# Optimization experiments

Measured on AMD Instinct MI355X. Metric: run time of the kernel, lower is better.

Reference implementation:

```python
import jax, jax.numpy as jnp
import numpy as np

B, S, H = 4, 1024, 2048
NQ, NKV, D = 32, 4, 128
EPS = 1e-6
THETA = 1e6


def setup_inputs() -> dict:
    key = jax.random.key(0)
    k1, k2, k3 = jax.random.split(key, 3)
    hidden = jax.random.normal(k1, (B, S, H), jnp.float32) * 0.02
    w_qkv = jax.random.normal(k2, (H, (NQ + 2 * NKV) * D), jnp.float32) * 0.02
    w_o = jax.random.normal(k3, (NQ * D, H), jnp.float32) * 0.02
    q_norm_w = jnp.ones((D,), jnp.float32)
    k_norm_w = jnp.ones((D,), jnp.float32)
    # rotary tables, broadcast to [B, S, D]
    inv_freq = 1.0 / (THETA ** (jnp.arange(0, D, 2, dtype=jnp.float32) / D))
    freqs = jnp.arange(S, dtype=jnp.float32)[:, None] * inv_freq[None, :]  # [S, D/2]
    emb = jnp.concatenate([freqs, freqs], axis=-1)  # [S, D]
    cos = jnp.broadcast_to(jnp.cos(emb)[None], (B, S, D))
    sin = jnp.broadcast_to(jnp.sin(emb)[None], (B, S, D))
    return {"hidden": hidden, "w_qkv": w_qkv, "w_o": w_o,
            "q_norm_w": q_norm_w, "k_norm_w": k_norm_w, "cos": cos, "sin": sin}


def _rms_norm(x, w):
    xf = x.astype(jnp.float32)
    var = jnp.mean(xf * xf, axis=-1, keepdims=True)
    return (w * (xf * jax.lax.rsqrt(var + EPS))).astype(x.dtype)


def _rotate_half(x):
    h = x.shape[-1] // 2
    return jnp.concatenate([-x[..., h:], x[..., :h]], axis=-1)


def reference(hidden, w_qkv, w_o, q_norm_w, k_norm_w, cos, sin):
    b, s, _ = hidden.shape
    qkv = jnp.einsum('bsh,he->bse', hidden, w_qkv)
    q = qkv[..., : NQ * D].reshape(b, s, NQ, D)
    k = qkv[..., NQ * D: (NQ + NKV) * D].reshape(b, s, NKV, D)
    v = qkv[..., (NQ + NKV) * D:].reshape(b, s, NKV, D)

    # per-head RMSNorm on Q and K
    q = _rms_norm(q, q_norm_w)
    k = _rms_norm(k, k_norm_w)

    # fused RoPE (rotate-half), cos/sin broadcast over heads
    c = cos[:, :, None, :]
    sn = sin[:, :, None, :]
    q = q * c + _rotate_half(q) * sn
    k = k * c + _rotate_half(k) * sn

    # GQA causal flash-attention (prefill, sparse_mode=3 -> causal)
    g = NQ // NKV
    qg = q.reshape(b, s, NKV, g, D)
    scale = 1.0 / jnp.sqrt(jnp.asarray(D, hidden.dtype))
    scores = jnp.einsum('bqkgd,bskd->bkgqs', qg, k) * scale  # [B,NKV,g,S,S]
    causal = jnp.tril(jnp.ones((s, s), bool))
    scores = jnp.where(causal[None, None, None], scores, jnp.finfo(scores.dtype).min)
    probs = jax.nn.softmax(scores, axis=-1)
    out = jnp.einsum('bkgqs,bskd->bqkgd', probs, v).reshape(b, s, NQ * D)
    return jnp.einsum('bse,eh->bsh', out, w_o)
```

## Files before the change

### kernel.cpp

```cpp
#include <hip/hip_runtime.h>

#define BB 4
#define SS 1024
#define HH 2048
#define NQH 32
#define NKVH 4
#define DD 128
#define EQKV 5120

typedef __attribute__((ext_vector_type(8))) short s8v;
typedef __attribute__((ext_vector_type(4))) short s4v;
typedef __attribute__((ext_vector_type(4))) float f4v;

__device__ __forceinline__ unsigned short f2bf(float f) {
  unsigned int u = __builtin_bit_cast(unsigned int, f);
  u += 0x7fffu + ((u >> 16) & 1u);
  return (unsigned short)(u >> 16);
}
__device__ __forceinline__ float bf2f(unsigned short s) {
  unsigned int u = ((unsigned int)s) << 16;
  return __builtin_bit_cast(float, u);
}

__device__ __forceinline__ void async16(unsigned short* lds, const unsigned short* g) {
  __builtin_amdgcn_global_load_lds(
      (const __attribute__((address_space(1))) unsigned int*)g,
      (__attribute__((address_space(3))) unsigned int*)lds, 16, 0, 0);
}


__global__ __launch_bounds__(256) void cvt_bf16(const float* __restrict__ in,
                                                unsigned short* __restrict__ out, int n) {
  int i = (blockIdx.x * 256 + threadIdx.x) * 4;
  if (i >= n) return;
  f4v v = *reinterpret_cast<const f4v*>(in + i);
  s4v o;
#pragma unroll
  for (int j = 0; j < 4; ++j) o[j] = (short)f2bf(v[j]);
  *reinterpret_cast<s4v*>(out + i) = o;
}

__global__ __launch_bounds__(256) void transpose_cvt(const float* __restrict__ in,
                                                     unsigned short* __restrict__ out,
                                                     int K, int N) {
  __shared__ unsigned short T[64][65];
  const int k0 = blockIdx.y * 64, n0 = blockIdx.x * 64;
  const int t = threadIdx.x;
  const int r = t >> 4, c4 = (t & 15) * 4;
#pragma unroll
  for (int i = 0; i < 4; ++i) {
    f4v v = *reinterpret_cast<const f4v*>(&in[(size_t)(k0 + r + i * 16) * N + n0 + c4]);
#pragma unroll
    for (int j = 0; j < 4; ++j) T[r + i * 16][c4 + j] = f2bf(v[j]);
  }
  __syncthreads();
#pragma unroll
  for (int i = 0; i < 4; ++i) {
    int n = r + i * 16;
    s4v o;
#pragma unroll
    for (int j = 0; j < 4; ++j) o[j] = (short)T[c4 + j][n];
    *reinterpret_cast<s4v*>(&out[(size_t)(n0 + n) * K + k0 + c4]) = o;
  }
}

__global__ __launch_bounds__(256) void vtrans(const unsigned short* __restrict__ qkv,
                                              unsigned short* __restrict__ Vt) {
  __shared__ unsigned short T[64][68];
  const int s0 = blockIdx.x * 64;
  const int d0 = blockIdx.y * 64;
  const int bk = blockIdx.z;
  const int b = bk >> 2, hkv = bk & 3;
  const int t = threadIdx.x;
  const int r = t >> 4, c4 = (t & 15) * 4;
  const unsigned short* src = qkv + (size_t)(b * SS + s0) * EQKV + (NQH + NKVH + hkv) * DD + d0;
#pragma unroll
  for (int i = 0; i < 4; ++i) {
    int s = r + i * 16;
    s4v v = *reinterpret_cast<const s4v*>(src + (size_t)s * EQKV + c4);
    *reinterpret_cast<s4v*>(&T[s][c4]) = v;
  }
  __syncthreads();
#pragma unroll
  for (int i = 0; i < 4; ++i) {
    int d = r + i * 16;
    s4v o;
#pragma unroll
    for (int j = 0; j < 4; ++j) o[j] = (short)T[c4 + j][d];
    *reinterpret_cast<s4v*>(&Vt[((size_t)bk * DD + d0 + d) * SS + s0 + c4]) = o;
  }
}

template <bool CF32>
__global__ __launch_bounds__(256) void gemm_bt(const unsigned short* __restrict__ A,
                                               const unsigned short* __restrict__ Bt,
                                               void* __restrict__ Cp,
                                               int M, int N, int K, int lda) {
  __shared__ unsigned short As[128 * 32];
  __shared__ unsigned short Bs[128 * 32];
  const int tid = threadIdx.x;
  const int ln = tid & 63, wv = tid >> 6;
  const int la = ln & 15, quad = ln >> 4;
  const int m0 = blockIdx.y * 128, n0 = blockIdx.x * 128;
  const int wm = (wv >> 1) * 64, wn = (wv & 1) * 64;
  f4v acc[4][4] = {};

  const int srow = wv * 16 + (ln >> 2);
  const int scol = (ln & 3) * 8;
  const unsigned short* Ab = A + (size_t)(m0 + srow) * lda + scol;
  const unsigned short* Bb = Bt + (size_t)(n0 + srow) * K + scol;
  unsigned short* AsW = &As[wv * 16 * 32];
  unsigned short* BsW = &Bs[wv * 16 * 32];

  for (int k0 = 0; k0 < K; k0 += 32) {
    async16(AsW,           Ab + k0);
    async16(AsW + 64 * 32, Ab + (size_t)64 * lda + k0);
    async16(BsW,           Bb + k0);
    async16(BsW + 64 * 32, Bb + (size_t)64 * K + k0);
    __syncthreads();
    s8v af[4], bf[4];
#pragma unroll
    for (int mi = 0; mi < 4; ++mi)
      af[mi] = *reinterpret_cast<const s8v*>(&As[(wm + mi * 16 + la) * 32 + quad * 8]);
#pragma unroll
    for (int ni = 0; ni < 4; ++ni)
      bf[ni] = *reinterpret_cast<const s8v*>(&Bs[(wn + ni * 16 + la) * 32 + quad * 8]);
#pragma unroll
    for (int mi = 0; mi < 4; ++mi)
#pragma unroll
      for (int ni = 0; ni < 4; ++ni)
        acc[mi][ni] = __builtin_amdgcn_mfma_f32_16x16x32_bf16(af[mi], bf[ni], acc[mi][ni], 0, 0, 0);
    __syncthreads();
  }
#pragma unroll
  for (int mi = 0; mi < 4; ++mi)
#pragma unroll
    for (int ni = 0; ni < 4; ++ni)
#pragma unroll
      for (int r = 0; r < 4; ++r) {
        int row = m0 + wm + mi * 16 + quad * 4 + r;
        int col = n0 + wn + ni * 16 + la;
        if constexpr (CF32) ((float*)Cp)[(size_t)row * N + col] = acc[mi][ni][r];
        else ((unsigned short*)Cp)[(size_t)row * N + col] = f2bf(acc[mi][ni][r]);
      }
}

__global__ __launch_bounds__(256) void attn2(unsigned short* __restrict__ qkv,
                                             const unsigned short* __restrict__ Vt) {
  const int idx = blockIdx.x;
  const int tile = 15 - (idx >> 7);
  const int h = idx & 31;
  const int b = (idx >> 5) & 3;
  const int hkv = h >> 3;
  const int tid = threadIdx.x;
  const int ln = tid & 63, w = tid >> 6;
  const int la = ln & 15, quad = ln >> 4;
  const int qr0 = tile * 64;
  __shared__ unsigned short Ks[64 * 128];
  __shared__ unsigned short Vts[128 * 64];
  __shared__ unsigned short Ps[4][16][64];

  const size_t rowb = (size_t)b * SS;
  s8v qf[4];
  {
    const unsigned short* qrow = qkv + (rowb + qr0 + w * 16 + la) * EQKV + h * DD;
#pragma unroll
    for (int t = 0; t < 4; ++t) qf[t] = *reinterpret_cast<const s8v*>(qrow + t * 32 + quad * 8);
  }
  const unsigned short* kcol = qkv + (NQH + hkv) * DD;
  const unsigned short* vtb = Vt + (size_t)(b * NKVH + hkv) * DD * SS;

  float m_[4], l_[4], al[4];
  f4v acc[8] = {};
#pragma unroll
  for (int r = 0; r < 4; ++r) { m_[r] = -1.0e30f; l_[r] = 0.f; }

  const float scale = 0.08838834764831845f;
  const int nkb = tile + 1;
  for (int kb = 0; kb < nkb; ++kb) {
    const int key0 = kb * 64;
    __syncthreads();
#pragma unroll
    for (int i = 0; i < 4; ++i) {
      int row = w * 16 + i * 4 + (ln >> 4);
      int chunk = (ln & 15) ^ (row & 15);
      async16(&Ks[(w * 16 + i * 4) * 128],
              kcol + (rowb + key0 + row) * EQKV + chunk * 8);
    }
#pragma unroll
    for (int i = 0; i < 4; ++i) {
      int row = w * 32 + i * 8 + (ln >> 3);
      int chunk = (ln & 7) ^ (ln >> 3);
      async16(&Vts[(w * 32 + i * 8) * 64],
              vtb + (size_t)row * SS + key0 + chunk * 8);
    }
    __syncthreads();
    f4v sc[4];
#pragma unroll
    for (int kt = 0; kt < 4; ++kt) {
      f4v z = {};
#pragma unroll
      for (int t = 0; t < 4; ++t) {
        s8v kf = *reinterpret_cast<const s8v*>(&Ks[(kt * 16 + la) * 128 + ((t * 4 + quad) ^ la) * 8]);
        z = __builtin_amdgcn_mfma_f32_16x16x32_bf16(qf[t], kf, z, 0, 0, 0);
      }
      sc[kt] = z;
    }
    const bool diag = (kb == nkb - 1);
#pragma unroll
    for (int r = 0; r < 4; ++r) {
      float v[4];
      if (diag) {
        int q = qr0 + w * 16 + quad * 4 + r;
#pragma unroll
        for (int kt = 0; kt < 4; ++kt)
          v[kt] = (key0 + kt * 16 + la <= q) ? sc[kt][r] * scale : -1.0e30f;
      } else {
#pragma unroll
        for (int kt = 0; kt < 4; ++kt) v[kt] = sc[kt][r] * scale;
      }
      float mx = fmaxf(fmaxf(v[0], v[1]), fmaxf(v[2], v[3]));
#pragma unroll
      for (int off = 8; off >= 1; off >>= 1) mx = fmaxf(mx, __shfl_xor(mx, off));
      float mnew = fmaxf(m_[r], mx);
      al[r] = __expf(m_[r] - mnew);
      m_[r] = mnew;
      float rsum = 0.f;
      const int row = quad * 4 + r;
#pragma unroll
      for (int kt = 0; kt < 4; ++kt) {
        float p = __expf(v[kt] - mnew);
        rsum += p;
        int col = kt * 16 + la;
        Ps[w][row][(((col >> 3) ^ (row & 7)) << 3) | (col & 7)] = f2bf(p);
      }
#pragma unroll
      for (int off = 8; off >= 1; off >>= 1) rsum += __shfl_xor(rsum, off);
      l_[r] = l_[r] * al[r] + rsum;
    }
#pragma unroll
    for (int nt = 0; nt < 8; ++nt)
#pragma unroll
      for (int r = 0; r < 4; ++r) acc[nt][r] *= al[r];
#pragma unroll
    for (int c = 0; c < 2; ++c) {
      s8v pf = *reinterpret_cast<const s8v*>(&Ps[w][la][(((c * 4 + quad) ^ (la & 7)) << 3)]);
#pragma unroll
      for (int nt = 0; nt < 8; ++nt) {
        s8v vf = *reinterpret_cast<const s8v*>(
            &Vts[(nt * 16 + la) * 64 + ((c * 4 + quad) ^ (la & 7)) * 8]);
        acc[nt] = __builtin_amdgcn_mfma_f32_16x16x32_bf16(pf, vf, acc[nt], 0, 0, 0);
      }
    }
  }
#pragma unroll
  for (int nt = 0; nt < 8; ++nt)
#pragma unroll
    for (int r = 0; r < 4; ++r) {
      int q = qr0 + w * 16 + quad * 4 + r;
      qkv[(rowb + q) * EQKV + h * DD + nt * 16 + la] = f2bf(acc[nt][r] / l_[r]);
    }
}

template <bool AF32, bool BF32, bool CF32>
__global__ __launch_bounds__(256) void gemm_t(const void* __restrict__ Ap,
                                              const void* __restrict__ Bp,
                                              void* __restrict__ Cp,
                                              int M, int N, int K, int lda) {
  __shared__ unsigned short As[64][40];
  __shared__ unsigned short Bs[64][40];
  const int tid  = threadIdx.x;
  const int lane = tid & 63;
  const int wave = tid >> 6;
  const int la   = lane & 15;
  const int quad = lane >> 4;
  const int m0 = blockIdx.y * 64;
  const int n0 = blockIdx.x * 64;
  const int wm = (wave >> 1) * 32;
  const int wn = (wave & 1) * 32;
  f4v acc[2][2] = {};
  const int ar = tid >> 2, ac = (tid & 3) * 8;
  const int bk = tid >> 3, bn = (tid & 7) * 8;
  for (int k0 = 0; k0 < K; k0 += 32) {
    s8v av;
    if constexpr (AF32) {
      const float* a = (const float*)Ap + (size_t)(m0 + ar) * lda + ac + k0;
      f4v v0 = *reinterpret_cast<const f4v*>(a);
      f4v v1 = *reinterpret_cast<const f4v*>(a + 4);
#pragma unroll
      for (int j = 0; j < 4; ++j) { av[j] = (short)f2bf(v0[j]); av[j + 4] = (short)f2bf(v1[j]); }
    } else {
      av = *reinterpret_cast<const s8v*>((const unsigned short*)Ap + (size_t)(m0 + ar) * lda + ac + k0);
    }
    unsigned short bvs[8];
    if constexpr (BF32) {
      const float* bp = (const float*)Bp + (size_t)(k0 + bk) * N + n0 + bn;
      f4v v0 = *reinterpret_cast<const f4v*>(bp);
      f4v v1 = *reinterpret_cast<const f4v*>(bp + 4);
#pragma unroll
      for (int j = 0; j < 4; ++j) { bvs[j] = f2bf(v0[j]); bvs[j + 4] = f2bf(v1[j]); }
    } else {
      s8v bv = *reinterpret_cast<const s8v*>((const unsigned short*)Bp + (size_t)(k0 + bk) * N + n0 + bn);
#pragma unroll
      for (int j = 0; j < 8; ++j) bvs[j] = (unsigned short)bv[j];
    }
    *reinterpret_cast<s8v*>(&As[ar][ac]) = av;
#pragma unroll
    for (int j = 0; j < 8; ++j) Bs[bn + j][bk] = bvs[j];
    __syncthreads();
#pragma unroll
    for (int mi = 0; mi < 2; ++mi) {
      s8v af = *reinterpret_cast<const s8v*>(&As[wm + mi * 16 + la][quad * 8]);
#pragma unroll
      for (int ni = 0; ni < 2; ++ni) {
        s8v bfr = *reinterpret_cast<const s8v*>(&Bs[wn + ni * 16 + la][quad * 8]);
        acc[mi][ni] = __builtin_amdgcn_mfma_f32_16x16x32_bf16(af, bfr, acc[mi][ni], 0, 0, 0);
      }
    }
    __syncthreads();
  }
#pragma unroll
  for (int mi = 0; mi < 2; ++mi)
#pragma unroll
    for (int ni = 0; ni < 2; ++ni)
#pragma unroll
      for (int r = 0; r < 4; ++r) {
        int row = m0 + wm + mi * 16 + quad * 4 + r;
        int col = n0 + wn + ni * 16 + la;
        if constexpr (CF32) ((float*)Cp)[(size_t)row * N + col] = acc[mi][ni][r];
        else ((unsigned short*)Cp)[(size_t)row * N + col] = f2bf(acc[mi][ni][r]);
      }
}

__global__ __launch_bounds__(64) void attn_slow(unsigned short* __restrict__ qkv) {
  const int tile = blockIdx.x;
  const int h = blockIdx.y;
  const int b = blockIdx.z;
  const int hkv = h >> 3;
  const int lane = threadIdx.x;
  const int la = lane & 15;
  const int quad = lane >> 4;
  const int qr0 = tile * 16;
  __shared__ unsigned short P[16][32];
  __shared__ unsigned short V[32][128];
  const size_t base = (size_t)b * SS * EQKV;
  s8v qf[4];
  {
    const unsigned short* qrow = qkv + base + (size_t)(qr0 + la) * EQKV + h * DD;
#pragma unroll
    for (int t = 0; t < 4; ++t)
      qf[t] = *reinterpret_cast<const s8v*>(qrow + t * 32 + quad * 8);
  }
  const unsigned short* kbase = qkv + base + (NQH + hkv) * DD;
  const unsigned short* vbase = qkv + base + (NQH + NKVH + hkv) * DD;
  float m[4], l[4], al[4];
  f4v acc[8] = {};
#pragma unroll
  for (int r = 0; r < 4; ++r) { m[r] = -1.0e30f; l[r] = 0.f; }
  const float scale = 0.08838834764831845f;
  const int nkb = (qr0 + 16 + 31) >> 5;
  for (int kb = 0; kb < nkb; ++kb) {
    const int key0 = kb * 32;
    __syncthreads();
#pragma unroll
    for (int i = 0; i < 8; ++i) {
      int c = i * 64 + lane;
      int row = c >> 4, col = (c & 15) * 8;
      *reinterpret_cast<s8v*>(&V[row][col]) =
          *reinterpret_cast<const s8v*>(vbase + (size_t)(key0 + row) * EQKV + col);
    }
    f4v s0 = {}, s1 = {};
#pragma unroll
    for (int t = 0; t < 4; ++t) {
      s8v k0f = *reinterpret_cast<const s8v*>(kbase + (size_t)(key0 + la) * EQKV + t * 32 + quad * 8);
      s8v k1f = *reinterpret_cast<const s8v*>(kbase + (size_t)(key0 + 16 + la) * EQKV + t * 32 + quad * 8);
      s0 = __builtin_amdgcn_mfma_f32_16x16x32_bf16(qf[t], k0f, s0, 0, 0, 0);
      s1 = __builtin_amdgcn_mfma_f32_16x16x32_bf16(qf[t], k1f, s1, 0, 0, 0);
    }
#pragma unroll
    for (int r = 0; r < 4; ++r) {
      int q = qr0 + quad * 4 + r;
      float v0 = (key0 + la <= q) ? s0[r] * scale : -1.0e30f;
      float v1 = (key0 + 16 + la <= q) ? s1[r] * scale : -1.0e30f;
      float mx = fmaxf(v0, v1);
#pragma unroll
      for (int off = 8; off >= 1; off >>= 1) mx = fmaxf(mx, __shfl_xor(mx, off));
      float mnew = fmaxf(m[r], mx);
      float p0 = __expf(v0 - mnew);
      float p1 = __expf(v1 - mnew);
      al[r] = __expf(m[r] - mnew);
      m[r] = mnew;
      float rsum = p0 + p1;
#pragma unroll
      for (int off = 8; off >= 1; off >>= 1) rsum += __shfl_xor(rsum, off);
      l[r] = l[r] * al[r] + rsum;
      P[quad * 4 + r][la] = f2bf(p0);
      P[quad * 4 + r][la + 16] = f2bf(p1);
    }
#pragma unroll
    for (int nt = 0; nt < 8; ++nt)
#pragma unroll
      for (int r = 0; r < 4; ++r) acc[nt][r] *= al[r];
    __syncthreads();
    s8v pf = *reinterpret_cast<const s8v*>(&P[la][quad * 8]);
#pragma unroll
    for (int nt = 0; nt < 8; ++nt) {
      s8v vf;
#pragma unroll
      for (int j = 0; j < 8; ++j)
        vf[j] = (short)V[quad * 8 + j][nt * 16 + la];
      acc[nt] = __builtin_amdgcn_mfma_f32_16x16x32_bf16(pf, vf, acc[nt], 0, 0, 0);
    }
  }
#pragma unroll
  for (int nt = 0; nt < 8; ++nt)
#pragma unroll
    for (int r = 0; r < 4; ++r) {
      int q = qr0 + quad * 4 + r;
      qkv[base + (size_t)q * EQKV + h * DD + nt * 16 + la] = f2bf(acc[nt][r] / l[r]);
    }
}

__global__ __launch_bounds__(256) void norm_rope(unsigned short* __restrict__ qkv,
                                                 const float* __restrict__ qw,
                                                 const float* __restrict__ kw,
                                                 const float* __restrict__ cosp,
                                                 const float* __restrict__ sinp) {
  const int h = blockIdx.x;
  const int bs = blockIdx.y * 4 + (threadIdx.x >> 6);
  const int s = bs & (SS - 1);
  const int lane = threadIdx.x & 63;
  const int d0 = lane * 2;
  unsigned short* p = qkv + (size_t)bs * EQKV + h * DD + d0;
  unsigned int u = *reinterpret_cast<const unsigned int*>(p);
  float x0 = bf2f((unsigned short)(u & 0xffff));
  float x1 = bf2f((unsigned short)(u >> 16));
  float ss = x0 * x0 + x1 * x1;
#pragma unroll
  for (int off = 32; off >= 1; off >>= 1) ss += __shfl_xor(ss, off);
  float rs = rsqrtf(ss * (1.0f / 128.0f) + 1e-6f);
  const float* w = (h < NQH) ? qw : kw;
  float n0 = x0 * rs * w[d0];
  float n1 = x1 * rs * w[d0 + 1];
  float o0 = __shfl_xor(n0, 32);
  float o1 = __shfl_xor(n1, 32);
  float r0 = (lane < 32) ? -o0 : o0;
  float r1 = (lane < 32) ? -o1 : o1;
  float c0 = cosp[(size_t)s * DD + d0], c1 = cosp[(size_t)s * DD + d0 + 1];
  float s0 = sinp[(size_t)s * DD + d0], s1 = sinp[(size_t)s * DD + d0 + 1];
  float y0 = n0 * c0 + r0 * s0;
  float y1 = n1 * c1 + r1 * s1;
  unsigned int outv = (unsigned int)f2bf(y0) | ((unsigned int)f2bf(y1) << 16);
  *reinterpret_cast<unsigned int*>(p) = outv;
}

extern "C" void kernel_launch(void* const* d_in, const int* in_sizes, int n_in,
                              void* d_out, int out_size, void* d_ws, size_t ws_size,
                              hipStream_t stream) {
  const float* hidden = (const float*)d_in[0];
  const float* w_qkv  = (const float*)d_in[1];
  const float* w_o    = (const float*)d_in[2];
  const float* q_w    = (const float*)d_in[3];
  const float* k_w    = (const float*)d_in[4];
  const float* cosp   = (const float*)d_in[5];
  const float* sinp   = (const float*)d_in[6];
  float* out = (float*)d_out;

  const int M = BB * SS;
  const size_t szHid  = (size_t)M * HH;
  const size_t szWqkv = (size_t)HH * EQKV;
  const size_t szWo   = (size_t)(NQH * DD) * HH;
  const size_t szQkv  = (size_t)M * EQKV;
  const size_t need = (szHid + szWqkv + szWo + szQkv) * sizeof(unsigned short);

  if (ws_size >= need) {
    unsigned short* hb16  = (unsigned short*)d_ws;
    unsigned short* wqkvT = hb16 + szHid;
    unsigned short* woT   = wqkvT + szWqkv;
    unsigned short* qkv   = woT + szWo;
    unsigned short* Vt    = hb16;

    cvt_bf16<<<(int)(szHid / 1024), 256, 0, stream>>>(hidden, hb16, (int)szHid);
    transpose_cvt<<<dim3(EQKV / 64, HH / 64), 256, 0, stream>>>(w_qkv, wqkvT, HH, EQKV);
    transpose_cvt<<<dim3(HH / 64, (NQH * DD) / 64), 256, 0, stream>>>(w_o, woT, NQH * DD, HH);

    gemm_bt<false><<<dim3(EQKV / 128, M / 128), 256, 0, stream>>>(
        hb16, wqkvT, qkv, M, EQKV, HH, HH);
    vtrans<<<dim3(SS / 64, DD / 64, BB * NKVH), 256, 0, stream>>>(qkv, Vt);
    norm_rope<<<dim3(NQH + NKVH, M / 4), 256, 0, stream>>>(qkv, q_w, k_w, cosp, sinp);
    attn2<<<2048, 256, 0, stream>>>(qkv, Vt);
    gemm_bt<true><<<dim3(HH / 128, M / 128), 256, 0, stream>>>(
        qkv, woT, out, M, HH, NQH * DD, EQKV);
  } else {
    unsigned short* qkvb = (unsigned short*)d_ws;
    for (int b = 0; b < BB; ++b) {
      const float* hb = hidden + (size_t)b * SS * HH;
      float* ob = out + (size_t)b * SS * HH;
      gemm_t<true, true, false><<<dim3(EQKV / 64, SS / 64), 256, 0, stream>>>(
          hb, w_qkv, qkvb, SS, EQKV, HH, HH);
      norm_rope<<<dim3(NQH + NKVH, SS / 4), 256, 0, stream>>>(qkvb, q_w, k_w, cosp, sinp);
      attn_slow<<<dim3(SS / 16, NQH, 1), 64, 0, stream>>>(qkvb);
      gemm_t<false, true, true><<<dim3(HH / 64, SS / 64), 256, 0, stream>>>(
          qkvb, w_o, ob, SS, HH, NQH * DD, EQKV);
    }
  }
}
```

Baseline: 501.5 us.

## Replace GEMM with 256x256 tile, 8-wave double-buffered pipelined kernel

Both bf16 GEMMs now use a new kernel with 256x256 output tiles, 8 waves per block, and 64-wide K steps double-buffered in LDS. Async global-to-LDS loads for the next tile are interleaved with the MFMA work under raised wave priority, and LDS chunks are XOR-swizzled to cut bank conflicts. The aim is to hide memory latency and raise arithmetic intensity compared with the single-buffered 128x128 kernel. The cost is 128KB of LDS per block. Grids shrink (the O-projection has only 128 blocks), which may leave CUs underused.

```diff
diff --git a/kernel.cpp b/kernel.cpp
--- a/kernel.cpp
+++ b/kernel.cpp
@@ -92,56 +92,103 @@
 }
 
 template <bool CF32>
-__global__ __launch_bounds__(256) void gemm_bt(const unsigned short* __restrict__ A,
-                                               const unsigned short* __restrict__ Bt,
-                                               void* __restrict__ Cp,
-                                               int M, int N, int K, int lda) {
-  __shared__ unsigned short As[128 * 32];
-  __shared__ unsigned short Bs[128 * 32];
+__global__ __launch_bounds__(512, 2) void gemm_bt8(const unsigned short* __restrict__ A,
+                                                   const unsigned short* __restrict__ Bt,
+                                                   void* __restrict__ Cp,
+                                                   int M, int N, int K, int lda) {
+  __shared__ unsigned short AsL[2][2][8192];
+  __shared__ unsigned short BsL[2][2][8192];
   const int tid = threadIdx.x;
-  const int ln = tid & 63, wv = tid >> 6;
+  const int ln = tid & 63, w = tid >> 6;
   const int la = ln & 15, quad = ln >> 4;
-  const int m0 = blockIdx.y * 128, n0 = blockIdx.x * 128;
-  const int wm = (wv >> 1) * 64, wn = (wv & 1) * 64;
-  f4v acc[4][4] = {};
-
-  const int srow = wv * 16 + (ln >> 2);
-  const int scol = (ln & 3) * 8;
-  const unsigned short* Ab = A + (size_t)(m0 + srow) * lda + scol;
-  const unsigned short* Bb = Bt + (size_t)(n0 + srow) * K + scol;
-  unsigned short* AsW = &As[wv * 16 * 32];
-  unsigned short* BsW = &Bs[wv * 16 * 32];
-
-  for (int k0 = 0; k0 < K; k0 += 32) {
-    async16(AsW,           Ab + k0);
-    async16(AsW + 64 * 32, Ab + (size_t)64 * lda + k0);
-    async16(BsW,           Bb + k0);
-    async16(BsW + 64 * 32, Bb + (size_t)64 * K + k0);
-    __syncthreads();
-    s8v af[4], bf[4];
-#pragma unroll
-    for (int mi = 0; mi < 4; ++mi)
-      af[mi] = *reinterpret_cast<const s8v*>(&As[(wm + mi * 16 + la) * 32 + quad * 8]);
-#pragma unroll
-    for (int ni = 0; ni < 4; ++ni)
-      bf[ni] = *reinterpret_cast<const s8v*>(&Bs[(wn + ni * 16 + la) * 32 + quad * 8]);
-#pragma unroll
-    for (int mi = 0; mi < 4; ++mi)
-#pragma unroll
-      for (int ni = 0; ni < 4; ++ni)
-        acc[mi][ni] = __builtin_amdgcn_mfma_f32_16x16x32_bf16(af[mi], bf[ni], acc[mi][ni], 0, 0, 0);
-    __syncthreads();
-  }
-#pragma unroll
-  for (int mi = 0; mi < 4; ++mi)
-#pragma unroll
-    for (int ni = 0; ni < 4; ++ni)
+  const int wr = w >> 2, wc = w & 3;
+  const int m0 = blockIdx.y * 256, n0 = blockIdx.x * 256;
+
+  f4v acc[8][4] = {};
+
+  const int schunk = (ln & 3) ^ ((ln >> 3) & 3);
+  const int r0 = w * 32 + (ln >> 2);
+  const int r1 = r0 + 16;
+  const unsigned short* pA0 = A + (size_t)(m0 + r0) * lda + schunk * 8;
+  const unsigned short* pA1 = A + (size_t)(m0 + r1) * lda + schunk * 8;
+  const unsigned short* pB0 = Bt + (size_t)(n0 + r0) * K + schunk * 8;
+  const unsigned short* pB1 = Bt + (size_t)(n0 + r1) * K + schunk * 8;
+
+  const int fch = (quad ^ ((la >> 1) & 3)) * 8;
+  const int arow = (wr * 128 + la) * 32;
+  const int brow = (wc * 64 + la) * 32;
+  const int NT = K / 64;
+
+#define STAGE_A(sb, kh, t)                                        \
+  async16(&AsL[sb][kh][w * 1024], pA0 + (t) * 64 + (kh) * 32);    \
+  async16(&AsL[sb][kh][w * 1024 + 512], pA1 + (t) * 64 + (kh) * 32);
+#define STAGE_B(sb, kh, t)                                        \
+  async16(&BsL[sb][kh][w * 1024], pB0 + (t) * 64 + (kh) * 32);    \
+  async16(&BsL[sb][kh][w * 1024 + 512], pB1 + (t) * 64 + (kh) * 32);
+
+#define HALF(buf, sbuf, kh, tn)                                                             \
+    _Pragma("unroll") for (int mf = 0; mf < 8; ++mf)                                        \
+      a[mf] = *reinterpret_cast<const s8v*>(&AsL[buf][kh][arow + mf * 512 + fch]);          \
+    b0 = *reinterpret_cast<const s8v*>(&BsL[buf][kh][brow + fch]);                          \
+    b1 = *reinterpret_cast<const s8v*>(&BsL[buf][kh][brow + 512 + fch]);                    \
+    STAGE_A(sbuf, kh, tn)                                                                   \
+    __builtin_amdgcn_s_barrier();                                                           \
+    __builtin_amdgcn_s_setprio(1);                                                          \
+    _Pragma("unroll") for (int mf = 0; mf < 8; ++mf) {                                      \
+      acc[mf][0] = __builtin_amdgcn_mfma_f32_16x16x32_bf16(a[mf], b0, acc[mf][0], 0, 0, 0); \
+      acc[mf][1] = __builtin_amdgcn_mfma_f32_16x16x32_bf16(a[mf], b1, acc[mf][1], 0, 0, 0); \
+    }                                                                                       \
+    __builtin_amdgcn_s_setprio(0);                                                          \
+    __builtin_amdgcn_s_barrier();                                                           \
+    b2 = *reinterpret_cast<const s8v*>(&BsL[buf][kh][brow + 1024 + fch]);                   \
+    b3 = *reinterpret_cast<const s8v*>(&BsL[buf][kh][brow + 1536 + fch]);                   \
+    STAGE_B(sbuf, kh, tn)                                                                   \
+    __builtin_amdgcn_s_barrier();                                                           \
+    __builtin_amdgcn_s_setprio(1);                                                          \
+    _Pragma("unroll") for (int mf = 0; mf < 8; ++mf) {                                      \
+      acc[mf][2] = __builtin_amdgcn_mfma_f32_16x16x32_bf16(a[mf], b2, acc[mf][2], 0, 0, 0); \
+      acc[mf][3] = __builtin_amdgcn_mfma_f32_16x16x32_bf16(a[mf], b3, acc[mf][3], 0, 0, 0); \
+    }                                                                                       \
+    __builtin_amdgcn_s_setprio(0);                                                          \
+    asm volatile("s_waitcnt vmcnt(4)" ::: "memory");                                        \
+    __builtin_amdgcn_s_barrier();
+
+#define TILE(buf, sbuf, tn) {                                                               \
+    s8v a[8], b0, b1, b2, b3;                                                               \
+    HALF(buf, sbuf, 0, tn)                                                                  \
+    HALF(buf, sbuf, 1, tn)                                                                  \
+  }
+
+  STAGE_A(0, 0, 0)
+  STAGE_B(0, 0, 0)
+  STAGE_A(0, 1, 0)
+  STAGE_B(0, 1, 0)
+  asm volatile("s_waitcnt vmcnt(4)" ::: "memory");
+  __builtin_amdgcn_s_barrier();
+
+  for (int it = 0; it < K / 128; ++it) {
+    const int t0 = it * 2;
+    const int t2 = (t0 + 2 < NT) ? t0 + 2 : NT - 1;
+    TILE(0, 1, t0 + 1)
+    TILE(1, 0, t2)
+  }
+  asm volatile("s_waitcnt vmcnt(0)" ::: "memory");
+
+#undef TILE
+#undef HALF
+#undef STAGE_A
+#undef STAGE_B
+
+#pragma unroll
+  for (int mf = 0; mf < 8; ++mf)
+#pragma unroll
+    for (int nf = 0; nf < 4; ++nf)
 #pragma unroll
       for (int r = 0; r < 4; ++r) {
-        int row = m0 + wm + mi * 16 + quad * 4 + r;
-        int col = n0 + wn + ni * 16 + la;
-        if constexpr (CF32) ((float*)Cp)[(size_t)row * N + col] = acc[mi][ni][r];
-        else ((unsigned short*)Cp)[(size_t)row * N + col] = f2bf(acc[mi][ni][r]);
+        int row = m0 + wr * 128 + mf * 16 + quad * 4 + r;
+        int col = n0 + wc * 64 + nf * 16 + la;
+        if constexpr (CF32) ((float*)Cp)[(size_t)row * N + col] = acc[mf][nf][r];
+        else ((unsigned short*)Cp)[(size_t)row * N + col] = f2bf(acc[mf][nf][r]);
       }
 }
 
@@ -484,12 +531,12 @@
     transpose_cvt<<<dim3(EQKV / 64, HH / 64), 256, 0, stream>>>(w_qkv, wqkvT, HH, EQKV);
     transpose_cvt<<<dim3(HH / 64, (NQH * DD) / 64), 256, 0, stream>>>(w_o, woT, NQH * DD, HH);
 
-    gemm_bt<false><<<dim3(EQKV / 128, M / 128), 256, 0, stream>>>(
+    gemm_bt8<false><<<dim3(EQKV / 256, M / 256), 512, 0, stream>>>(
         hb16, wqkvT, qkv, M, EQKV, HH, HH);
     vtrans<<<dim3(SS / 64, DD / 64, BB * NKVH), 256, 0, stream>>>(qkv, Vt);
     norm_rope<<<dim3(NQH + NKVH, M / 4), 256, 0, stream>>>(qkv, q_w, k_w, cosp, sinp);
     attn2<<<2048, 256, 0, stream>>>(qkv, Vt);
-    gemm_bt<true><<<dim3(HH / 128, M / 128), 256, 0, stream>>>(
+    gemm_bt8<true><<<dim3(HH / 256, M / 256), 512, 0, stream>>>(
         qkv, woT, out, M, HH, NQH * DD, EQKV);
   } else {
     unsigned short* qkvb = (unsigned short*)d_ws;
```

New measurement: 561.8 us. +12.0%, slower.

## Replace GEMM with deep 6-stage async LDS ring pipeline and larger tiles

Applied to the files above, without the earlier changes.

Replaces the single-buffered 128x128 bf16 GEMM with a 512-thread 128x256 tile kernel that keeps a six-slot LDS ring, prefetching five K-steps ahead with vmcnt-based waits and one barrier per step. It adds an XOR swizzle on LDS chunks to cut bank conflicts, raises wave priority around the MFMA block, and remaps block IDs for L2 locality. The aim is to hide global load latency behind MFMA work in both projection GEMMs. The cost is large LDS use (144 KB), which limits occupancy to one block per CU, plus reliance on hand-counted outstanding loads.

```diff
diff --git a/kernel.cpp b/kernel.cpp
--- a/kernel.cpp
+++ b/kernel.cpp
@@ -92,56 +92,96 @@
 }
 
 template <bool CF32>
-__global__ __launch_bounds__(256) void gemm_bt(const unsigned short* __restrict__ A,
-                                               const unsigned short* __restrict__ Bt,
-                                               void* __restrict__ Cp,
-                                               int M, int N, int K, int lda) {
-  __shared__ unsigned short As[128 * 32];
-  __shared__ unsigned short Bs[128 * 32];
+__global__ __launch_bounds__(512) void gemm_deep(const unsigned short* __restrict__ A,
+                                                 const unsigned short* __restrict__ Bt,
+                                                 void* __restrict__ Cp,
+                                                 int M, int N, int K, int lda) {
+  __shared__ unsigned short RING[6][12288];
   const int tid = threadIdx.x;
-  const int ln = tid & 63, wv = tid >> 6;
+  const int ln = tid & 63, w = tid >> 6;
   const int la = ln & 15, quad = ln >> 4;
-  const int m0 = blockIdx.y * 128, n0 = blockIdx.x * 128;
-  const int wm = (wv >> 1) * 64, wn = (wv & 1) * 64;
+  const int wr = w >> 2, wc = w & 3;
+
+  const int G = gridDim.x, cpx = G >> 3;
+  const int swz = (blockIdx.x & 7) * cpx + (blockIdx.x >> 3);
+  const int ytiles = M >> 7;
+  const int by = swz % ytiles, bx = swz / ytiles;
+  const int m0 = by * 128, n0 = bx * 256;
+
   f4v acc[4][4] = {};
 
-  const int srow = wv * 16 + (ln >> 2);
-  const int scol = (ln & 3) * 8;
-  const unsigned short* Ab = A + (size_t)(m0 + srow) * lda + scol;
-  const unsigned short* Bb = Bt + (size_t)(n0 + srow) * K + scol;
-  unsigned short* AsW = &As[wv * 16 * 32];
-  unsigned short* BsW = &Bs[wv * 16 * 32];
-
-  for (int k0 = 0; k0 < K; k0 += 32) {
-    async16(AsW,           Ab + k0);
-    async16(AsW + 64 * 32, Ab + (size_t)64 * lda + k0);
-    async16(BsW,           Bb + k0);
-    async16(BsW + 64 * 32, Bb + (size_t)64 * K + k0);
-    __syncthreads();
-    s8v af[4], bf[4];
-#pragma unroll
-    for (int mi = 0; mi < 4; ++mi)
-      af[mi] = *reinterpret_cast<const s8v*>(&As[(wm + mi * 16 + la) * 32 + quad * 8]);
-#pragma unroll
-    for (int ni = 0; ni < 4; ++ni)
-      bf[ni] = *reinterpret_cast<const s8v*>(&Bs[(wn + ni * 16 + la) * 32 + quad * 8]);
-#pragma unroll
-    for (int mi = 0; mi < 4; ++mi)
-#pragma unroll
-      for (int ni = 0; ni < 4; ++ni)
-        acc[mi][ni] = __builtin_amdgcn_mfma_f32_16x16x32_bf16(af[mi], bf[ni], acc[mi][ni], 0, 0, 0);
-    __syncthreads();
-  }
-#pragma unroll
-  for (int mi = 0; mi < 4; ++mi)
-#pragma unroll
-    for (int ni = 0; ni < 4; ++ni)
+  const int srow = tid >> 2;
+  const int schunk = (tid & 3) ^ ((tid >> 3) & 3);
+  const int rb0 = w * 32 + (ln >> 2);
+  const unsigned short* pA  = A  + (size_t)(m0 + srow) * lda + schunk * 8;
+  const unsigned short* pB0 = Bt + (size_t)(n0 + rb0) * K   + schunk * 8;
+  const unsigned short* pB1 = pB0 + (size_t)16 * K;
+  unsigned short* ldsA = nullptr;
+
+  const int fch = (quad ^ ((la >> 1) & 3)) * 8;
+  const int ar = (wr * 64 + la) * 32;
+  const int br = 4096 + (wc * 64 + la) * 32;
+
+#define STAGE(s, koff)                                          \
+  async16(&RING[s][w * 512], pA + (koff));                      \
+  async16(&RING[s][4096 + w * 1024], pB0 + (koff));             \
+  async16(&RING[s][4096 + w * 1024 + 512], pB1 + (koff));
+
+#pragma unroll
+  for (int pp = 0; pp < 5; ++pp) { STAGE(pp, pp * 32) }
+  asm volatile("s_waitcnt vmcnt(12)" ::: "memory");
+  __builtin_amdgcn_s_barrier();
+
+  const int NP = K >> 5;
+  const int kend = K - 32;
+  int u = 0, su = 5, ks = 160;
+  for (int p = 0; p < NP; ++p) {
+    s8v a0 = *reinterpret_cast<const s8v*>(&RING[u][ar + fch]);
+    s8v a1 = *reinterpret_cast<const s8v*>(&RING[u][ar + 512 + fch]);
+    s8v a2 = *reinterpret_cast<const s8v*>(&RING[u][ar + 1024 + fch]);
+    s8v a3 = *reinterpret_cast<const s8v*>(&RING[u][ar + 1536 + fch]);
+    s8v b0 = *reinterpret_cast<const s8v*>(&RING[u][br + fch]);
+    s8v b1 = *reinterpret_cast<const s8v*>(&RING[u][br + 512 + fch]);
+    s8v b2 = *reinterpret_cast<const s8v*>(&RING[u][br + 1024 + fch]);
+    s8v b3 = *reinterpret_cast<const s8v*>(&RING[u][br + 1536 + fch]);
+    STAGE(su, ks)
+    __builtin_amdgcn_s_setprio(1);
+    acc[0][0] = __builtin_amdgcn_mfma_f32_16x16x32_bf16(a0, b0, acc[0][0], 0, 0, 0);
+    acc[0][1] = __builtin_amdgcn_mfma_f32_16x16x32_bf16(a0, b1, acc[0][1], 0, 0, 0);
+    acc[0][2] = __builtin_amdgcn_mfma_f32_16x16x32_bf16(a0, b2, acc[0][2], 0, 0, 0);
+    acc[0][3] = __builtin_amdgcn_mfma_f32_16x16x32_bf16(a0, b3, acc[0][3], 0, 0, 0);
+    acc[1][0] = __builtin_amdgcn_mfma_f32_16x16x32_bf16(a1, b0, acc[1][0], 0, 0, 0);
+    acc[1][1] = __builtin_amdgcn_mfma_f32_16x16x32_bf16(a1, b1, acc[1][1], 0, 0, 0);
+    acc[1][2] = __builtin_amdgcn_mfma_f32_16x16x32_bf16(a1, b2, acc[1][2], 0, 0, 0);
+    acc[1][3] = __builtin_amdgcn_mfma_f32_16x16x32_bf16(a1, b3, acc[1][3], 0, 0, 0);
+    acc[2][0] = __builtin_amdgcn_mfma_f32_16x16x32_bf16(a2, b0, acc[2][0], 0, 0, 0);
+    acc[2][1] = __builtin_amdgcn_mfma_f32_16x16x32_bf16(a2, b1, acc[2][1], 0, 0, 0);
+    acc[2][2] = __builtin_amdgcn_mfma_f32_16x16x32_bf16(a2, b2, acc[2][2], 0, 0, 0);
+    acc[2][3] = __builtin_amdgcn_mfma_f32_16x16x32_bf16(a2, b3, acc[2][3], 0, 0, 0);
+    acc[3][0] = __builtin_amdgcn_mfma_f32_16x16x32_bf16(a3, b0, acc[3][0], 0, 0, 0);
+    acc[3][1] = __builtin_amdgcn_mfma_f32_16x16x32_bf16(a3, b1, acc[3][1], 0, 0, 0);
+    acc[3][2] = __builtin_amdgcn_mfma_f32_16x16x32_bf16(a3, b2, acc[3][2], 0, 0, 0);
+    acc[3][3] = __builtin_amdgcn_mfma_f32_16x16x32_bf16(a3, b3, acc[3][3], 0, 0, 0);
+    __builtin_amdgcn_s_setprio(0);
+    asm volatile("s_waitcnt vmcnt(12)" ::: "memory");
+    __builtin_amdgcn_s_barrier();
+    u = (u == 5) ? 0 : u + 1;
+    su = (su == 5) ? 0 : su + 1;
+    ks = (ks < kend) ? ks + 32 : ks;
+  }
+  asm volatile("s_waitcnt vmcnt(0)" ::: "memory");
+#undef STAGE
+
+#pragma unroll
+  for (int mf = 0; mf < 4; ++mf)
+#pragma unroll
+    for (int nf = 0; nf < 4; ++nf)
 #pragma unroll
       for (int r = 0; r < 4; ++r) {
-        int row = m0 + wm + mi * 16 + quad * 4 + r;
-        int col = n0 + wn + ni * 16 + la;
-        if constexpr (CF32) ((float*)Cp)[(size_t)row * N + col] = acc[mi][ni][r];
-        else ((unsigned short*)Cp)[(size_t)row * N + col] = f2bf(acc[mi][ni][r]);
+        int row = m0 + wr * 64 + mf * 16 + quad * 4 + r;
+        int col = n0 + wc * 64 + nf * 16 + la;
+        if constexpr (CF32) ((float*)Cp)[(size_t)row * N + col] = acc[mf][nf][r];
+        else ((unsigned short*)Cp)[(size_t)row * N + col] = f2bf(acc[mf][nf][r]);
       }
 }
 
@@ -484,12 +524,12 @@
     transpose_cvt<<<dim3(EQKV / 64, HH / 64), 256, 0, stream>>>(w_qkv, wqkvT, HH, EQKV);
     transpose_cvt<<<dim3(HH / 64, (NQH * DD) / 64), 256, 0, stream>>>(w_o, woT, NQH * DD, HH);
 
-    gemm_bt<false><<<dim3(EQKV / 128, M / 128), 256, 0, stream>>>(
+    gemm_deep<false><<<(EQKV / 256) * (M / 128), 512, 0, stream>>>(
         hb16, wqkvT, qkv, M, EQKV, HH, HH);
     vtrans<<<dim3(SS / 64, DD / 64, BB * NKVH), 256, 0, stream>>>(qkv, Vt);
     norm_rope<<<dim3(NQH + NKVH, M / 4), 256, 0, stream>>>(qkv, q_w, k_w, cosp, sinp);
     attn2<<<2048, 256, 0, stream>>>(qkv, Vt);
-    gemm_bt<true><<<dim3(HH / 128, M / 128), 256, 0, stream>>>(
+    gemm_deep<true><<<(HH / 256) * (M / 128), 512, 0, stream>>>(
         qkv, woT, out, M, HH, NQH * DD, EQKV);
   } else {
     unsigned short* qkvb = (unsigned short*)d_ws;
```

New measurement: 468.3 us. 1.07x faster.
